# Kernel optimization log

Hardware: AMD Instinct MI355X
Metric: run time of the kernel (lower is better)

Reference implementation:

```python
import jax, jax.numpy as jnp
import numpy as np

B, L, IN_DIM, D, H = 4, 1024, 256, 512, 8
DH = D // H
LARGE_NEG = -10000.0
LN_EPS = 1e-5


def _layernorm(x, g, b):
    mu = jnp.mean(x, axis=-1, keepdims=True)
    var = jnp.mean((x - mu) ** 2, axis=-1, keepdims=True)
    return (x - mu) * jax.lax.rsqrt(var + LN_EPS) * g + b


def setup_inputs() -> dict:
    key = jax.random.key(0)
    ks = jax.random.split(key, 16)
    s = 0.02
    return {
        "x": jax.random.normal(ks[0], (B, L, IN_DIM), jnp.float32),
        "attention_mask": jax.random.bernoulli(ks[1], 0.5, (B, L, L)),
        "adjacency_matrix": jax.random.uniform(ks[2], (B, L, L), jnp.float32),
        "W_fuse": jax.random.normal(ks[3], (D, IN_DIM), jnp.float32) * s,
        "b_fuse": jnp.zeros((D,), jnp.float32),
        "in_proj_w": jax.random.normal(ks[4], (3 * D, D), jnp.float32) * s,
        "in_proj_b": jnp.zeros((3 * D,), jnp.float32),
        "out_w": jax.random.normal(ks[5], (D, D), jnp.float32) * s,
        "out_b": jnp.zeros((D,), jnp.float32),
        "ln1_g": jnp.ones((D,), jnp.float32),
        "ln1_b": jnp.zeros((D,), jnp.float32),
        "ln2_g": jnp.ones((D,), jnp.float32),
        "ln2_b": jnp.zeros((D,), jnp.float32),
        "W1": jax.random.normal(ks[6], (4 * D, D), jnp.float32) * s,
        "b1": jnp.zeros((4 * D,), jnp.float32),
        "W2": jax.random.normal(ks[7], (D, 4 * D), jnp.float32) * s,
        "b2": jnp.zeros((D,), jnp.float32),
        "log_scale": jnp.array(0.0, jnp.float32),  # log(adj_bias_strength=1.0)
    }


def reference(x, attention_mask, adjacency_matrix, W_fuse, b_fuse, in_proj_w,
              in_proj_b, out_w, out_b, ln1_g, ln1_b, ln2_g, ln2_b,
              W1, b1, W2, b2, log_scale):
    # fuse projection (in_dim != d_model)
    x = jnp.einsum("bli,di->bld", x, W_fuse) + b_fuse

    # ensure_self_loops_in_mask: unmask diagonal of fully-masked rows
    eye = jnp.eye(L, dtype=bool)
    row_all = jnp.all(attention_mask, axis=-1)  # [B, L]
    mask = attention_mask & ~(eye[None, :, :] & row_all[:, :, None])

    # additive attention bias: large_neg where masked + scaled clipped adjacency
    bias = jnp.where(mask, LARGE_NEG, 0.0) + \
        jnp.exp(log_scale) * jnp.clip(adjacency_matrix, 0.0, 1.0)  # [B, L, L]

    # --- attention block (pre-norm) ---
    x_norm = _layernorm(x, ln1_g, ln1_b)
    qkv = jnp.einsum("bld,ed->ble", x_norm, in_proj_w) + in_proj_b
    q, k, v = jnp.split(qkv, 3, axis=-1)
    q = q.reshape(B, L, H, DH).transpose(0, 2, 1, 3)  # [B,H,L,DH]
    k = k.reshape(B, L, H, DH).transpose(0, 2, 1, 3)
    v = v.reshape(B, L, H, DH).transpose(0, 2, 1, 3)
    scores = jnp.einsum("bhqd,bhkd->bhqk", q, k) / np.sqrt(DH) + bias[:, None]
    probs = jax.nn.softmax(scores, axis=-1)
    ctx = jnp.einsum("bhqk,bhkd->bhqd", probs, v)
    ctx = ctx.transpose(0, 2, 1, 3).reshape(B, L, D)
    attn_out = jnp.einsum("bld,ed->ble", ctx, out_w) + out_b
    x = x + attn_out

    # --- FFN block (pre-norm) ---
    x_norm = _layernorm(x, ln2_g, ln2_b)
    h = jax.nn.gelu(jnp.einsum("bld,fd->blf", x_norm, W1) + b1, approximate=False)
    ff = jnp.einsum("blf,df->bld", h, W2) + b2
    return x + ff
```

## Files before the change

kernel.cpp:

```cpp
#include <hip/hip_runtime.h>
#include <math.h>

typedef unsigned short UST;
typedef __attribute__((ext_vector_type(8))) short bf16x8;
typedef __attribute__((ext_vector_type(4))) float f32x4;

#define BB 4
#define LL 1024
#define IND 256
#define DD 512
#define HH 8
#define FFD 2048
#define NT (BB*LL)

__device__ __forceinline__ float bf2f(UST u){ return __uint_as_float(((unsigned)u)<<16); }
__device__ __forceinline__ UST f2bf(float f){
  unsigned u = __float_as_uint(f);
  u += 0x7FFFu + ((u>>16)&1u);
  return (UST)(u>>16);
}
__device__ __forceinline__ float ldF(const void* p, long i, int isf32){
  return isf32 ? ((const float*)p)[i] : bf2f(((const UST*)p)[i]);
}
__device__ __forceinline__ bool ldMask(const void* p, long i, int fm){
  if (fm==0) return ((const int*)p)[i] != 0;
  if (fm==1) return ((const unsigned char*)p)[i] != 0;
  if (fm==2) return ((const UST*)p)[i] != 0;
  return ((const float*)p)[i] != 0.f;
}
__device__ __forceinline__ f32x4 mfma16(bf16x8 a, bf16x8 b, f32x4 c){
  return __builtin_amdgcn_mfma_f32_16x16x32_bf16(a, b, c, 0, 0, 0);
}
__device__ __forceinline__ void gld16(const void* g, void* l){
  __builtin_amdgcn_global_load_lds((const __attribute__((address_space(1))) unsigned int*)g,
                                   (__attribute__((address_space(3))) unsigned int*)l, 16, 0, 0);
}

__global__ void detect_k(int* flags, const UST* xh, const unsigned int* mw){
  if (threadIdx.x != 0) return;
  int f32 = 0;
  for (int i = 0; i < 128; ++i){
    int e = (xh[i] >> 7) & 0xFF;
    if (e >= 140) f32 = 1;
  }
  int allW01=1, allHalf=1, allWordF=1, allByte=1;
  for (int i = 0; i < 64; ++i){
    unsigned v = mw[i];
    if (v > 1u) allW01 = 0;
    unsigned lo = v & 0xFFFFu, hi = v >> 16;
    if (!((lo==0u||lo==0x3F80u)&&(hi==0u||hi==0x3F80u))) allHalf = 0;
    if (!(v==0u || v==0x3F800000u)) allWordF = 0;
    #pragma unroll
    for (int bs=0; bs<32; bs+=8){ unsigned bt=(v>>bs)&0xFFu; if (bt>1u) allByte=0; }
  }
  int fm;
  if (allW01) fm = 0;
  else if (allHalf) fm = allWordF ? 3 : 2;
  else if (allByte) fm = 1;
  else fm = 0;
  flags[0] = f32;
  flags[1] = fm;
}

struct CvtArgs { const void* src[11]; UST* dst[11]; int n[11]; };
__global__ __launch_bounds__(256) void cvt_k(const int* flags, CvtArgs a){
  int ti = blockIdx.y;
  int n = a.n[ti];
  long i8 = ((long)blockIdx.x*256 + threadIdx.x)*8;
  if (i8 >= n) return;
  const void* s = a.src[ti]; UST* d = a.dst[ti];
  if (flags[0]){
    const float4* sf = (const float4*)s;
    float4 a0 = sf[i8>>2], a1 = sf[(i8>>2)+1];
    UST o[8] = { f2bf(a0.x),f2bf(a0.y),f2bf(a0.z),f2bf(a0.w),
                 f2bf(a1.x),f2bf(a1.y),f2bf(a1.z),f2bf(a1.w) };
    *(int4*)(d+i8) = *(const int4*)o;
  } else {
    ((int4*)d)[i8>>3] = ((const int4*)s)[i8>>3];
  }
}

__global__ __launch_bounds__(256) void bias_k(const int* flags, const void* mask,
                                              const void* adj, const void* lsp, UST* biasOut){
  int fF = flags[0], fM = flags[1];
  int row = blockIdx.x;
  int i = row & (LL-1);
  long base = (long)row * LL;
  int t = threadIdx.x;
  bool mv[4]; int my = 1;
  #pragma unroll
  for (int k = 0; k < 4; ++k){
    mv[k] = ldMask(mask, base + t + k*256, fM);
    my &= mv[k] ? 1 : 0;
  }
  int wa = __all(my);
  __shared__ int sAll[4];
  int w = t >> 6;
  if ((t & 63) == 0) sAll[w] = wa;
  __syncthreads();
  int rowAll = sAll[0] & sAll[1] & sAll[2] & sAll[3];
  float es = expf(ldF(lsp, 0, fF));
  #pragma unroll
  for (int k = 0; k < 4; ++k){
    int j = t + k*256;
    float a = ldF(adj, base + j, fF);
    a = fminf(fmaxf(a, 0.f), 1.f);
    bool eff = mv[k] && !((rowAll != 0) && (j == i));
    float bz = (eff ? -10000.f : 0.f) + es * a;
    biasOut[base + j] = f2bf(bz);
  }
}

template<int NI, int ACT, int RES, int OUTMODE>
__global__ __launch_bounds__(256) void gemm2_k(const int* flags,
    const UST* __restrict__ A, const UST* __restrict__ Bw, const UST* __restrict__ bias,
    const float* __restrict__ resid, void* Cout, int M, int N, int K){
  constexpr int TN = 32*NI;
  __shared__ UST sA[128*32];
  __shared__ UST sB[TN*32];
  int t = threadIdx.x, w = t>>6, lane = t&63, l15 = lane&15, qd = lane>>4;
  int m0 = blockIdx.x*128, n0 = blockIdx.y*TN;
  int wm = (w&1)*64, wn = (w>>1)*(NI*16);
  f32x4 acc[4][NI];
  #pragma unroll
  for (int mi=0; mi<4; ++mi)
    #pragma unroll
    for (int ni=0; ni<NI; ++ni){ acc[mi][ni][0]=0;acc[mi][ni][1]=0;acc[mi][ni][2]=0;acc[mi][ni][3]=0; }
  int arow = t>>2, acol = (t&3)*8;
  const UST* aSrc = A + (long)(m0+arow)*K + acol;
  const UST* bSrc = Bw + (long)(n0+arow)*K + acol;
  char* ldsA0 = (char*)sA + (w*64)*16;
  char* ldsA1 = (char*)sA + (256 + w*64)*16;
  char* ldsB0 = (char*)sB + (w*64)*16;
  char* ldsB1 = (char*)sB + (256 + w*64)*16;
  for (int k0 = 0; k0 < K; k0 += 32){
    __syncthreads();
    gld16(aSrc + k0, ldsA0);
    gld16(aSrc + 64*K + k0, ldsA1);
    gld16(bSrc + k0, ldsB0);
    if (NI == 4) gld16(bSrc + 64*K + k0, ldsB1);
    __syncthreads();
    bf16x8 afr[4], bfr[NI];
    #pragma unroll
    for (int mi=0; mi<4; ++mi) afr[mi] = *(const bf16x8*)&sA[(wm + mi*16 + l15)*32 + qd*8];
    #pragma unroll
    for (int ni=0; ni<NI; ++ni) bfr[ni] = *(const bf16x8*)&sB[(wn + ni*16 + l15)*32 + qd*8];
    #pragma unroll
    for (int mi=0; mi<4; ++mi)
      #pragma unroll
      for (int ni=0; ni<NI; ++ni)
        acc[mi][ni] = mfma16(afr[mi], bfr[ni], acc[mi][ni]);
  }
  int outF32 = (OUTMODE==1) || (OUTMODE==2 && flags[0]);
  #pragma unroll
  for (int mi=0; mi<4; ++mi){
    #pragma unroll
    for (int ni=0; ni<NI; ++ni){
      int gc = n0 + wn + ni*16 + l15;
      float bv = bf2f(bias[gc]);
      #pragma unroll
      for (int r=0; r<4; ++r){
        int grow = m0 + wm + mi*16 + qd*4 + r;
        float c = acc[mi][ni][r] + bv;
        if (ACT) c = 0.5f*c*(1.f+erff(c*0.70710678118654752f));
        long oi = (long)grow*N + gc;
        if (RES) c += resid[oi];
        if (outF32) ((float*)Cout)[oi] = c;
        else ((UST*)Cout)[oi] = f2bf(c);
      }
    }
  }
}

__global__ __launch_bounds__(256) void ln_k(const int* flags, const float* xin,
    const void* gp, const void* bp, UST* xout){
  int fF = flags[0];
  int row = blockIdx.x, t = threadIdx.x;
  const float* xr = xin + (long)row * DD;
  float v0 = xr[t], v1 = xr[t+256];
  float s = v0+v1, q = v0*v0 + v1*v1;
  #pragma unroll
  for (int off=1; off<64; off<<=1){ s += __shfl_xor(s,off,64); q += __shfl_xor(q,off,64); }
  __shared__ float rs[4], rq[4];
  int w = t>>6;
  if ((t&63)==0){ rs[w]=s; rq[w]=q; }
  __syncthreads();
  float S = rs[0]+rs[1]+rs[2]+rs[3];
  float Q = rq[0]+rq[1]+rq[2]+rq[3];
  float mean = S * (1.f/DD);
  float var  = fmaxf(Q * (1.f/DD) - mean*mean, 0.f);
  float ri = rsqrtf(var + 1e-5f);
  float g0 = ldF(gp, t, fF), b0 = ldF(bp, t, fF);
  float g1 = ldF(gp, t+256, fF), b1 = ldF(bp, t+256, fF);
  xout[(long)row*DD + t]     = f2bf((v0-mean)*ri*g0 + b0);
  xout[(long)row*DD + t+256] = f2bf((v1-mean)*ri*g1 + b1);
}

__global__ __launch_bounds__(256) void attn_k(const UST* qkv, const UST* bias, UST* ctx){
  int qt = blockIdx.x, bh = blockIdx.y;
  int b = bh >> 3, h = bh & 7;
  int q0 = qt * 64;
  int t = threadIdx.x, w = t>>6, lane = t&63, l15 = lane&15, qd = lane>>4;
  __shared__ UST sK[64*72], sV[64*72], sBias[64*72];
  __shared__ UST sP[4][16*72];
  long qrow = ((long)(b*LL + q0 + w*16 + l15))*1536 + h*64;
  bf16x8 qf0 = *(const bf16x8*)(qkv + qrow + qd*8);
  bf16x8 qf1 = *(const bf16x8*)(qkv + qrow + 32 + qd*8);
  f32x4 o[4]; float mr_[4], lr_[4];
  #pragma unroll
  for (int i=0;i<4;i++){ o[i][0]=0;o[i][1]=0;o[i][2]=0;o[i][3]=0; mr_[i]=-1e30f; lr_[i]=0.f; }
  int rr = t>>2, c4 = (t&3)*16;
  for (int kt = 0; kt < 16; ++kt){
    long kvb = ((long)(b*LL + kt*64 + rr))*1536 + h*64 + c4;
    int4 kv0 = *(const int4*)(qkv + kvb + 512);
    int4 kv1 = *(const int4*)(qkv + kvb + 520);
    int4 vv0 = *(const int4*)(qkv + kvb + 1024);
    int4 vv1 = *(const int4*)(qkv + kvb + 1032);
    long bb = ((long)b<<20) + (long)(q0+rr)*LL + kt*64 + c4;
    int4 bz0 = *(const int4*)(bias + bb);
    int4 bz1 = *(const int4*)(bias + bb + 8);
    __syncthreads();
    *(int4*)&sK[rr*72 + c4]      = kv0;
    *(int4*)&sK[rr*72 + c4 + 8]  = kv1;
    *(int4*)&sBias[rr*72 + c4]     = bz0;
    *(int4*)&sBias[rr*72 + c4 + 8] = bz1;
    union { int4 v; UST u[8]; } u0, u1;
    u0.v = vv0; u1.v = vv1;
    #pragma unroll
    for (int i=0;i<8;i++){ sV[(c4+i)*72 + rr] = u0.u[i]; sV[(c4+8+i)*72 + rr] = u1.u[i]; }
    __syncthreads();
    f32x4 s4[4];
    #pragma unroll
    for (int i=0;i<4;i++){ s4[i][0]=0;s4[i][1]=0;s4[i][2]=0;s4[i][3]=0; }
    #pragma unroll
    for (int ni=0; ni<4; ++ni){
      bf16x8 kf0 = *(const bf16x8*)&sK[(ni*16+l15)*72 + qd*8];
      bf16x8 kf1 = *(const bf16x8*)&sK[(ni*16+l15)*72 + 32 + qd*8];
      s4[ni] = mfma16(qf0, kf0, s4[ni]);
      s4[ni] = mfma16(qf1, kf1, s4[ni]);
    }
    float sv[4][4];
    #pragma unroll
    for (int ni=0; ni<4; ++ni){
      #pragma unroll
      for (int r=0; r<4; ++r){
        int ql = w*16 + qd*4 + r;
        float bzv = bf2f(sBias[ql*72 + ni*16 + l15]);
        sv[ni][r] = s4[ni][r]*0.125f + bzv;
      }
    }
    float alpha[4];
    #pragma unroll
    for (int r=0; r<4; ++r){
      float mcur = fmaxf(fmaxf(sv[0][r],sv[1][r]), fmaxf(sv[2][r],sv[3][r]));
      #pragma unroll
      for (int off=1; off<16; off<<=1) mcur = fmaxf(mcur, __shfl_xor(mcur,off,64));
      float mn = fmaxf(mr_[r], mcur);
      alpha[r] = expf(mr_[r]-mn);
      mr_[r] = mn;
      float psum = 0.f;
      #pragma unroll
      for (int ni=0; ni<4; ++ni){ float p = expf(sv[ni][r]-mn); sv[ni][r]=p; psum += p; }
      #pragma unroll
      for (int off=1; off<16; off<<=1) psum += __shfl_xor(psum,off,64);
      lr_[r] = lr_[r]*alpha[r] + psum;
    }
    #pragma unroll
    for (int dn=0; dn<4; ++dn){
      #pragma unroll
      for (int r=0; r<4; ++r) o[dn][r] *= alpha[r];
    }
    #pragma unroll
    for (int ni=0; ni<4; ++ni){
      #pragma unroll
      for (int r=0; r<4; ++r) sP[w][(qd*4+r)*72 + ni*16 + l15] = f2bf(sv[ni][r]);
    }
    bf16x8 pf0 = *(const bf16x8*)&sP[w][l15*72 + qd*8];
    bf16x8 pf1 = *(const bf16x8*)&sP[w][l15*72 + 32 + qd*8];
    #pragma unroll
    for (int dn=0; dn<4; ++dn){
      bf16x8 vf0 = *(const bf16x8*)&sV[(dn*16+l15)*72 + qd*8];
      bf16x8 vf1 = *(const bf16x8*)&sV[(dn*16+l15)*72 + 32 + qd*8];
      o[dn] = mfma16(pf0, vf0, o[dn]);
      o[dn] = mfma16(pf1, vf1, o[dn]);
    }
  }
  #pragma unroll
  for (int dn=0; dn<4; ++dn){
    #pragma unroll
    for (int r=0; r<4; ++r){
      long oi = ((long)(b*LL + q0 + w*16 + qd*4 + r))*DD + h*64 + dn*16 + l15;
      ctx[oi] = f2bf(o[dn][r] * (1.f/lr_[r]));
    }
  }
}

extern "C" void kernel_launch(void* const* d_in, const int* in_sizes, int n_in,
                              void* d_out, int out_size, void* d_ws, size_t ws_size,
                              hipStream_t stream){
  char* ws = (char*)d_ws;
  size_t o = 0;
  auto alloc = [&](size_t b){ size_t r = o; o += (b + 255) & ~(size_t)255; return r; };
  int*   flags = (int*)(ws + alloc(256));
  size_t biasOff = alloc(8UL<<20);
  size_t qkvOff  = alloc(12UL<<20);
  UST* biasC = (UST*)(ws + biasOff);
  UST* qkv   = (UST*)(ws + qkvOff);
  UST* hb    = (UST*)(ws + biasOff);
  UST* xbf   = (UST*)(ws + alloc(2UL<<20));
  UST* wfuse = (UST*)(ws + alloc(131072*2));
  UST* bfuse = (UST*)(ws + alloc(1024));
  UST* ipw   = (UST*)(ws + alloc(786432*2));
  UST* ipb   = (UST*)(ws + alloc(3072*2));
  UST* outw  = (UST*)(ws + alloc(262144*2));
  UST* outb  = (UST*)(ws + alloc(1024));
  UST* w1    = (UST*)(ws + alloc(1048576*2));
  UST* b1    = (UST*)(ws + alloc(4096*2));
  UST* w2    = (UST*)(ws + alloc(1048576*2));
  UST* b2    = (UST*)(ws + alloc(1024));
  float* xf  = (float*)(ws + alloc((size_t)NT*DD*4));
  UST* xn    = (UST*)(ws + alloc((size_t)NT*DD*2));
  UST* ctx   = (UST*)(ws + alloc((size_t)NT*DD*2));
  float* x2  = (float*)(ws + alloc((size_t)NT*DD*4));

  detect_k<<<1, 64, 0, stream>>>(flags, (const UST*)d_in[0], (const unsigned int*)d_in[1]);

  CvtArgs ca;
  const int srcIdx[11] = {0,3,4,5,6,7,8,13,14,15,16};
  UST* dsts[11] = {xbf,wfuse,bfuse,ipw,ipb,outw,outb,w1,b1,w2,b2};
  const int ns[11] = {NT*IND, DD*IND, DD, 3*DD*DD, 3*DD, DD*DD, DD, FFD*DD, FFD, DD*FFD, DD};
  for (int i=0;i<11;i++){ ca.src[i]=d_in[srcIdx[i]]; ca.dst[i]=dsts[i]; ca.n[i]=ns[i]; }
  cvt_k<<<dim3(512,11), 256, 0, stream>>>(flags, ca);

  bias_k<<<BB*LL, 256, 0, stream>>>(flags, d_in[1], d_in[2], d_in[17], biasC);

  gemm2_k<2,0,0,1><<<dim3(32,8), 256, 0, stream>>>(flags, xbf, wfuse, bfuse, nullptr, xf, NT, DD, IND);
  ln_k<<<NT, 256, 0, stream>>>(flags, xf, d_in[9], d_in[10], xn);
  gemm2_k<4,0,0,0><<<dim3(32,12), 256, 0, stream>>>(flags, xn, ipw, ipb, nullptr, qkv, NT, 3*DD, DD);
  attn_k<<<dim3(LL/64, BB*HH), 256, 0, stream>>>(qkv, biasC, ctx);
  gemm2_k<2,0,1,1><<<dim3(32,8), 256, 0, stream>>>(flags, ctx, outw, outb, xf, x2, NT, DD, DD);
  ln_k<<<NT, 256, 0, stream>>>(flags, x2, d_in[11], d_in[12], xn);
  gemm2_k<4,1,0,0><<<dim3(32,16), 256, 0, stream>>>(flags, xn, w1, b1, nullptr, hb, NT, FFD, DD);
  gemm2_k<2,0,1,2><<<dim3(32,8), 256, 0, stream>>>(flags, hb, w2, b2, x2, d_out, NT, DD, FFD);
}
```

Baseline: 308.5 us.

## Load K/V/bias directly from global in attention, pre-transpose V, remove block syncs

Adds a repack kernel that writes V transposed per (batch, head) so the P·V MFMA fragments can be read with vector loads straight from global memory. The attention kernel stops staging K, V and bias through shared memory, which removes both __syncthreads per key tile and the scalar transposed LDS stores for V. It also reorders block indices so the four batches of a head sit in neighbouring blocks, switches to exp2f with a folded log2e, and rewrites the flag detection as a wave-parallel vote. The cost is an extra kernel launch plus a 4 MB transpose pass, and global/L2 traffic goes up because each wave now fetches K and V on its own instead of sharing one tile.

Result: no change. 310.8 us (+0.8%).

```diff
diff --git a/kernel.cpp b/kernel.cpp
--- a/kernel.cpp
+++ b/kernel.cpp
@@ -37,29 +37,20 @@
 }
 
 __global__ void detect_k(int* flags, const UST* xh, const unsigned int* mw){
-  if (threadIdx.x != 0) return;
-  int f32 = 0;
-  for (int i = 0; i < 128; ++i){
-    int e = (xh[i] >> 7) & 0xFF;
-    if (e >= 140) f32 = 1;
-  }
-  int allW01=1, allHalf=1, allWordF=1, allByte=1;
-  for (int i = 0; i < 64; ++i){
-    unsigned v = mw[i];
-    if (v > 1u) allW01 = 0;
-    unsigned lo = v & 0xFFFFu, hi = v >> 16;
-    if (!((lo==0u||lo==0x3F80u)&&(hi==0u||hi==0x3F80u))) allHalf = 0;
-    if (!(v==0u || v==0x3F800000u)) allWordF = 0;
-    #pragma unroll
-    for (int bs=0; bs<32; bs+=8){ unsigned bt=(v>>bs)&0xFFu; if (bt>1u) allByte=0; }
-  }
-  int fm;
-  if (allW01) fm = 0;
-  else if (allHalf) fm = allWordF ? 3 : 2;
-  else if (allByte) fm = 1;
-  else fm = 0;
-  flags[0] = f32;
-  flags[1] = fm;
+  int lane = threadIdx.x & 63;
+  int e0 = (xh[lane] >> 7) & 0xFF;
+  int e1 = (xh[64+lane] >> 7) & 0xFF;
+  int f32 = __any((e0 >= 140) || (e1 >= 140)) ? 1 : 0;
+  unsigned v = mw[lane];
+  int w01   = __all(v <= 1u) ? 1 : 0;
+  unsigned lo = v & 0xFFFFu, hi = v >> 16;
+  int half  = __all((lo==0u||lo==0x3F80u) && (hi==0u||hi==0x3F80u)) ? 1 : 0;
+  int wordF = __all(v==0u || v==0x3F800000u) ? 1 : 0;
+  int byteB = __all((v & 0xFEFEFEFEu) == 0u) ? 1 : 0;
+  if (lane == 0){
+    flags[0] = f32;
+    flags[1] = w01 ? 0 : (half ? (wordF ? 3 : 2) : (byteB ? 1 : 0));
+  }
 }
 
 struct CvtArgs { const void* src[11]; UST* dst[11]; int n[11]; };
@@ -196,59 +187,65 @@
   xout[(long)row*DD + t+256] = f2bf((v1-mean)*ri*g1 + b1);
 }
 
-__global__ __launch_bounds__(256) void attn_k(const UST* qkv, const UST* bias, UST* ctx){
-  int qt = blockIdx.x, bh = blockIdx.y;
+__global__ __launch_bounds__(256) void repack_v(const UST* __restrict__ qkv, UST* __restrict__ vT){
+  int id = blockIdx.x;
+  int bh = id & 31, qt = id >> 5;
   int b = bh >> 3, h = bh & 7;
-  int q0 = qt * 64;
+  int t = threadIdx.x, w = t >> 6, lane = t & 63;
+  int token = qt*64 + lane;
+  const UST* src = qkv + ((long)(b*LL + token))*1536 + 1024 + h*64;
+  #pragma unroll
+  for (int c = 0; c < 2; ++c){
+    int ch = w*2 + c;
+    union { int4 v; UST u[8]; } uu;
+    uu.v = *(const int4*)(src + ch*8);
+    #pragma unroll
+    for (int i = 0; i < 8; ++i)
+      vT[((long)(bh*64 + ch*8 + i))*LL + token] = uu.u[i];
+  }
+}
+
+__global__ __launch_bounds__(256) void attn_k(const UST* __restrict__ qkv,
+    const UST* __restrict__ vT, const UST* __restrict__ bias, UST* __restrict__ ctx){
+  int id = blockIdx.x;
+  int b = id & 3, h = (id>>2) & 7, qt = id >> 5;
+  int bh = b*HH + h;
+  int q0 = qt*64;
   int t = threadIdx.x, w = t>>6, lane = t&63, l15 = lane&15, qd = lane>>4;
-  __shared__ UST sK[64*72], sV[64*72], sBias[64*72];
-  __shared__ UST sP[4][16*72];
-  long qrow = ((long)(b*LL + q0 + w*16 + l15))*1536 + h*64;
-  bf16x8 qf0 = *(const bf16x8*)(qkv + qrow + qd*8);
-  bf16x8 qf1 = *(const bf16x8*)(qkv + qrow + 32 + qd*8);
+  __shared__ UST sP[4][16*80];
+  UST* myP = &sP[w][0];
+  const UST* qrow = qkv + ((long)(b*LL + q0 + w*16 + l15))*1536 + h*64;
+  bf16x8 qf0 = *(const bf16x8*)(qrow + qd*8);
+  bf16x8 qf1 = *(const bf16x8*)(qrow + 32 + qd*8);
+  const UST* bptr[4];
+  #pragma unroll
+  for (int r=0;r<4;++r)
+    bptr[r] = bias + ((long)b<<20) + (long)(q0 + w*16 + qd*4 + r)*LL + l15;
+  const UST* kBase = qkv + (long)b*LL*1536 + 512 + h*64;
+  const UST* vBase = vT + (long)bh*64*LL;
   f32x4 o[4]; float mr_[4], lr_[4];
   #pragma unroll
   for (int i=0;i<4;i++){ o[i][0]=0;o[i][1]=0;o[i][2]=0;o[i][3]=0; mr_[i]=-1e30f; lr_[i]=0.f; }
-  int rr = t>>2, c4 = (t&3)*16;
+  const float LOG2E = 1.44269504f;
   for (int kt = 0; kt < 16; ++kt){
-    long kvb = ((long)(b*LL + kt*64 + rr))*1536 + h*64 + c4;
-    int4 kv0 = *(const int4*)(qkv + kvb + 512);
-    int4 kv1 = *(const int4*)(qkv + kvb + 520);
-    int4 vv0 = *(const int4*)(qkv + kvb + 1024);
-    int4 vv1 = *(const int4*)(qkv + kvb + 1032);
-    long bb = ((long)b<<20) + (long)(q0+rr)*LL + kt*64 + c4;
-    int4 bz0 = *(const int4*)(bias + bb);
-    int4 bz1 = *(const int4*)(bias + bb + 8);
-    __syncthreads();
-    *(int4*)&sK[rr*72 + c4]      = kv0;
-    *(int4*)&sK[rr*72 + c4 + 8]  = kv1;
-    *(int4*)&sBias[rr*72 + c4]     = bz0;
-    *(int4*)&sBias[rr*72 + c4 + 8] = bz1;
-    union { int4 v; UST u[8]; } u0, u1;
-    u0.v = vv0; u1.v = vv1;
-    #pragma unroll
-    for (int i=0;i<8;i++){ sV[(c4+i)*72 + rr] = u0.u[i]; sV[(c4+8+i)*72 + rr] = u1.u[i]; }
-    __syncthreads();
+    int k0 = kt*64;
     f32x4 s4[4];
     #pragma unroll
     for (int i=0;i<4;i++){ s4[i][0]=0;s4[i][1]=0;s4[i][2]=0;s4[i][3]=0; }
     #pragma unroll
     for (int ni=0; ni<4; ++ni){
-      bf16x8 kf0 = *(const bf16x8*)&sK[(ni*16+l15)*72 + qd*8];
-      bf16x8 kf1 = *(const bf16x8*)&sK[(ni*16+l15)*72 + 32 + qd*8];
+      const UST* kp = kBase + (long)(k0 + ni*16 + l15)*1536 + qd*8;
+      bf16x8 kf0 = *(const bf16x8*)kp;
+      bf16x8 kf1 = *(const bf16x8*)(kp + 32);
       s4[ni] = mfma16(qf0, kf0, s4[ni]);
       s4[ni] = mfma16(qf1, kf1, s4[ni]);
     }
     float sv[4][4];
     #pragma unroll
-    for (int ni=0; ni<4; ++ni){
-      #pragma unroll
-      for (int r=0; r<4; ++r){
-        int ql = w*16 + qd*4 + r;
-        float bzv = bf2f(sBias[ql*72 + ni*16 + l15]);
-        sv[ni][r] = s4[ni][r]*0.125f + bzv;
-      }
-    }
+    for (int ni=0; ni<4; ++ni)
+      #pragma unroll
+      for (int r=0; r<4; ++r)
+        sv[ni][r] = fmaf(s4[ni][r], 0.125f, bf2f(bptr[r][k0 + ni*16]));
     float alpha[4];
     #pragma unroll
     for (int r=0; r<4; ++r){
@@ -256,31 +253,34 @@
       #pragma unroll
       for (int off=1; off<16; off<<=1) mcur = fmaxf(mcur, __shfl_xor(mcur,off,64));
       float mn = fmaxf(mr_[r], mcur);
-      alpha[r] = expf(mr_[r]-mn);
+      alpha[r] = exp2f((mr_[r]-mn)*LOG2E);
       mr_[r] = mn;
+      float mn2 = mn*LOG2E;
       float psum = 0.f;
       #pragma unroll
-      for (int ni=0; ni<4; ++ni){ float p = expf(sv[ni][r]-mn); sv[ni][r]=p; psum += p; }
+      for (int ni=0; ni<4; ++ni){
+        float p = exp2f(fmaf(sv[ni][r], LOG2E, -mn2));
+        sv[ni][r] = p; psum += p;
+      }
       #pragma unroll
       for (int off=1; off<16; off<<=1) psum += __shfl_xor(psum,off,64);
       lr_[r] = lr_[r]*alpha[r] + psum;
     }
     #pragma unroll
+    for (int dn=0; dn<4; ++dn)
+      #pragma unroll
+      for (int r=0; r<4; ++r) o[dn][r] *= alpha[r];
+    #pragma unroll
+    for (int ni=0; ni<4; ++ni)
+      #pragma unroll
+      for (int r=0; r<4; ++r) myP[(qd*4+r)*80 + ni*16 + l15] = f2bf(sv[ni][r]);
+    bf16x8 pf0 = *(const bf16x8*)&myP[l15*80 + qd*8];
+    bf16x8 pf1 = *(const bf16x8*)&myP[l15*80 + 32 + qd*8];
+    #pragma unroll
     for (int dn=0; dn<4; ++dn){
-      #pragma unroll
-      for (int r=0; r<4; ++r) o[dn][r] *= alpha[r];
-    }
-    #pragma unroll
-    for (int ni=0; ni<4; ++ni){
-      #pragma unroll
-      for (int r=0; r<4; ++r) sP[w][(qd*4+r)*72 + ni*16 + l15] = f2bf(sv[ni][r]);
-    }
-    bf16x8 pf0 = *(const bf16x8*)&sP[w][l15*72 + qd*8];
-    bf16x8 pf1 = *(const bf16x8*)&sP[w][l15*72 + 32 + qd*8];
-    #pragma unroll
-    for (int dn=0; dn<4; ++dn){
-      bf16x8 vf0 = *(const bf16x8*)&sV[(dn*16+l15)*72 + qd*8];
-      bf16x8 vf1 = *(const bf16x8*)&sV[(dn*16+l15)*72 + 32 + qd*8];
+      const UST* vp = vBase + (long)(dn*16 + l15)*LL + k0 + qd*8;
+      bf16x8 vf0 = *(const bf16x8*)vp;
+      bf16x8 vf1 = *(const bf16x8*)(vp + 32);
       o[dn] = mfma16(pf0, vf0, o[dn]);
       o[dn] = mfma16(pf1, vf1, o[dn]);
     }
@@ -307,6 +307,7 @@
   UST* biasC = (UST*)(ws + biasOff);
   UST* qkv   = (UST*)(ws + qkvOff);
   UST* hb    = (UST*)(ws + biasOff);
+  UST* vT    = (UST*)(ws + alloc(4UL<<20));
   UST* xbf   = (UST*)(ws + alloc(2UL<<20));
   UST* wfuse = (UST*)(ws + alloc(131072*2));
   UST* bfuse = (UST*)(ws + alloc(1024));
@@ -337,7 +338,8 @@
   gemm2_k<2,0,0,1><<<dim3(32,8), 256, 0, stream>>>(flags, xbf, wfuse, bfuse, nullptr, xf, NT, DD, IND);
   ln_k<<<NT, 256, 0, stream>>>(flags, xf, d_in[9], d_in[10], xn);
   gemm2_k<4,0,0,0><<<dim3(32,12), 256, 0, stream>>>(flags, xn, ipw, ipb, nullptr, qkv, NT, 3*DD, DD);
-  attn_k<<<dim3(LL/64, BB*HH), 256, 0, stream>>>(qkv, biasC, ctx);
+  repack_v<<<512, 256, 0, stream>>>(qkv, vT);
+  attn_k<<<512, 256, 0, stream>>>(qkv, vT, biasC, ctx);
   gemm2_k<2,0,1,1><<<dim3(32,8), 256, 0, stream>>>(flags, ctx, outw, outb, xf, x2, NT, DD, DD);
   ln_k<<<NT, 256, 0, stream>>>(flags, x2, d_in[11], d_in[12], xn);
   gemm2_k<4,1,0,0><<<dim3(32,16), 256, 0, stream>>>(flags, xn, w1, b1, nullptr, hb, NT, FFD, DD);
```
